# Kernel optimization log

Measured on AMD Instinct MI355X. Metric: run time of the kernel, lower is better.

## Reference

```python
import jax, jax.numpy as jnp
import numpy as np

B, N, DIM, H, E = 2, 2048, 1024, 16, 8
HD = DIM // H
SCALE = HD ** -0.5


def setup_inputs() -> dict:
    key = jax.random.key(0)
    ks = jax.random.split(key, 6)
    s = DIM ** -0.5
    return {
        "x": jax.random.normal(ks[0], (B, N, DIM), dtype=jnp.float32),
        "w_qkv": jax.random.normal(ks[1], (3 * DIM, DIM), dtype=jnp.float32) * s,
        "b_qkv": jnp.zeros((3 * DIM,), dtype=jnp.float32),
        "w_proj": jax.random.normal(ks[2], (DIM, DIM), dtype=jnp.float32) * s,
        "b_proj": jnp.zeros((DIM,), dtype=jnp.float32),
        "rel_pos": jax.random.normal(ks[3], (1, H, E, E), dtype=jnp.float32),
    }


def reference(x, w_qkv, b_qkv, w_proj, b_proj, rel_pos):
    tpe = N // E  # tokens per entity (tile count)
    # qkv: [B,N,3*DIM] -> [3,B,H,N,HD]
    qkv = (jnp.einsum("bnc,dc->bnd", x, w_qkv) + b_qkv)
    qkv = qkv.reshape(B, N, 3, H, HD).transpose(2, 0, 3, 1, 4)
    q, k, v = qkv[0], qkv[1], qkv[2]
    attn = jnp.einsum("bhnd,bhmd->bhnm", q, k) * SCALE
    # torch .repeat tiles the ExE bias: bias[i,j] = rel_pos[i % E, j % E]
    rel_bias = jnp.tile(rel_pos, (B, 1, tpe, tpe))
    attn = jax.nn.softmax(attn + rel_bias, axis=-1)
    out = jnp.einsum("bhnm,bhmd->bhnd", attn, v)
    out = out.transpose(0, 2, 1, 3).reshape(B, N, DIM)
    return jnp.einsum("bnc,dc->bnd", out, w_proj) + b_proj
```

## Files before the change

### kernel.cpp

```cpp
#include <hip/hip_runtime.h>
#include <hip/hip_bf16.h>
#include <stdint.h>

#define B_ 2
#define N_ 2048
#define DIM_ 1024
#define H_ 16
#define HD_ 64
#define NT_ 32

typedef __attribute__((ext_vector_type(8))) short short8;
typedef __attribute__((ext_vector_type(4))) float f32x4;

__device__ __forceinline__ unsigned short f2bf(float f) {
  __bf16 h = (__bf16)f;
  return __builtin_bit_cast(unsigned short, h);
}

__device__ __forceinline__ void gload_lds16(const void* g, void* l) {
  __builtin_amdgcn_global_load_lds(
      (const __attribute__((address_space(1))) unsigned int*)g,
      (__attribute__((address_space(3))) unsigned int*)l,
      16, 0, 0);
}

#define XN4_ 1048576
#define WQ4_ 786432
__global__ __launch_bounds__(256) void cvt_all_kernel(
    const float4* __restrict__ x, const float4* __restrict__ wq,
    const float4* __restrict__ wp,
    ushort4* __restrict__ xb, ushort4* __restrict__ wqb, ushort4* __restrict__ wpb) {
  int i = blockIdx.x * 256 + threadIdx.x;
  const float4* src;
  ushort4* dst;
  if (i < XN4_) {
    src = x + i; dst = xb + i;
  } else if (i < XN4_ + WQ4_) {
    src = wq + (i - XN4_); dst = wqb + (i - XN4_);
  } else {
    src = wp + (i - XN4_ - WQ4_); dst = wpb + (i - XN4_ - WQ4_);
  }
  float4 v = *src;
  ushort4 o;
  o.x = f2bf(v.x); o.y = f2bf(v.y); o.z = f2bf(v.z); o.w = f2bf(v.w);
  *dst = o;
}

__device__ __forceinline__ void gemm128_mainloop(
    const ushort* __restrict__ A, const ushort* __restrict__ Bw, int K,
    int bm, int bn, ushort* As, ushort* Bs, f32x4 acc[4][4]) {
  const int tid = threadIdx.x;
  const int lane = tid & 63;
  const int w = tid >> 6, wr = w >> 1, wc = w & 1;
  const int fr = lane & 15, fq = lane >> 4;
  const int srow = tid >> 3, scol = (tid & 7) * 8;

  const ushort* Ag = A + (size_t)(bm * 128 + srow) * K + scol;
  const ushort* Bg = Bw + (size_t)(bn * 128 + srow) * K + scol;
  ushort* Asd = As + tid * 8;
  ushort* Bsd = Bs + tid * 8;

  for (int kt = 0; kt < K; kt += 64) {
    __syncthreads();
#pragma unroll
    for (int c = 0; c < 4; ++c) {
      gload_lds16(Ag + (size_t)(c * 32) * K + kt, Asd + c * 2048);
      gload_lds16(Bg + (size_t)(c * 32) * K + kt, Bsd + c * 2048);
    }
    __syncthreads();

    short8 af[2][4], bf[2][4];
#pragma unroll
    for (int kk = 0; kk < 2; ++kk) {
#pragma unroll
      for (int mi = 0; mi < 4; ++mi)
        af[kk][mi] = *(const short8*)&As[(wr * 64 + mi * 16 + fr) * 64 + kk * 32 + fq * 8];
#pragma unroll
      for (int ni = 0; ni < 4; ++ni)
        bf[kk][ni] = *(const short8*)&Bs[(wc * 64 + ni * 16 + fr) * 64 + kk * 32 + fq * 8];
    }
#pragma unroll
    for (int kk = 0; kk < 2; ++kk)
#pragma unroll
      for (int mi = 0; mi < 4; ++mi)
#pragma unroll
        for (int ni = 0; ni < 4; ++ni)
          acc[mi][ni] = __builtin_amdgcn_mfma_f32_16x16x32_bf16(
              af[kk][mi], bf[kk][ni], acc[mi][ni], 0, 0, 0);
  }
}

__global__ __launch_bounds__(256) void gemm_qkv_kernel(
    const ushort* __restrict__ xb, const ushort* __restrict__ wqkv,
    const float* __restrict__ bqkv,
    ushort* __restrict__ qo, ushort* __restrict__ ko, ushort* __restrict__ vo) {
  __shared__ ushort As[128 * 64];
  __shared__ ushort Bs[128 * 64];
  f32x4 acc[4][4] = {};
  const int bn = blockIdx.x, bm = blockIdx.y;
  gemm128_mainloop(xb, wqkv, DIM_, bm, bn, As, Bs, acc);

  const int tid = threadIdx.x, lane = tid & 63;
  const int w = tid >> 6, wr = w >> 1, wc = w & 1;
  const int fr = lane & 15, fq = lane >> 4;
#pragma unroll
  for (int mi = 0; mi < 4; ++mi) {
#pragma unroll
    for (int ni = 0; ni < 4; ++ni) {
      int col = bn * 128 + wc * 64 + ni * 16 + fr;
      int i3 = col >> 10, h = (col >> 6) & 15, hd = col & 63;
      float bias = bqkv[col];
      int m0 = bm * 128 + wr * 64 + mi * 16 + fq * 4;
      int b = m0 >> 11, n = m0 & 2047;
      if (i3 == 2) {
        ushort4 o;
        o.x = f2bf(acc[mi][ni][0] + bias);
        o.y = f2bf(acc[mi][ni][1] + bias);
        o.z = f2bf(acc[mi][ni][2] + bias);
        o.w = f2bf(acc[mi][ni][3] + bias);
        *(ushort4*)&vo[((size_t)((b * H_ + h) * HD_ + hd)) * N_ + n] = o;
      } else {
        ushort* base = (i3 == 0) ? qo : ko;
#pragma unroll
        for (int r = 0; r < 4; ++r)
          base[((size_t)(b * H_ + h) * N_ + n + r) * HD_ + hd] = f2bf(acc[mi][ni][r] + bias);
      }
    }
  }
}

__global__ __launch_bounds__(256) void gemm_proj_kernel(
    const ushort* __restrict__ ao, const ushort* __restrict__ wp,
    const float* __restrict__ bp, float* __restrict__ out) {
  __shared__ ushort As[128 * 64];
  __shared__ ushort Bs[128 * 64];
  f32x4 acc[4][4] = {};
  const int bn = blockIdx.x, bm = blockIdx.y;
  gemm128_mainloop(ao, wp, DIM_, bm, bn, As, Bs, acc);

  const int tid = threadIdx.x, lane = tid & 63;
  const int w = tid >> 6, wr = w >> 1, wc = w & 1;
  const int fr = lane & 15, fq = lane >> 4;
#pragma unroll
  for (int mi = 0; mi < 4; ++mi) {
#pragma unroll
    for (int ni = 0; ni < 4; ++ni) {
      int col = bn * 128 + wc * 64 + ni * 16 + fr;
      float bias = bp[col];
#pragma unroll
      for (int r = 0; r < 4; ++r) {
        int m = bm * 128 + wr * 64 + mi * 16 + fq * 4 + r;
        out[(size_t)m * DIM_ + col] = acc[mi][ni][r] + bias;
      }
    }
  }
}

__global__ __launch_bounds__(256) void attn_kernel(
    const ushort* __restrict__ Qg, const ushort* __restrict__ Kg,
    const ushort* __restrict__ Vtg, const float* __restrict__ rel,
    ushort* __restrict__ outb) {
  __shared__ ushort Ks[2][64 * 64];
  __shared__ ushort Vs[2][64 * 64];
  __shared__ ushort Ps[4][2][16 * 64];

  const int bid = blockIdx.x;
  const int xcd = bid & 7, idx = bid >> 3;
  const int bh = xcd * 4 + (idx >> 4);
  const int q0 = (idx & 15) * 128;
  const int h = bh & 15;
  const int tid = threadIdx.x, lane = tid & 63, w = tid >> 6;
  const int fr = lane & 15, fq = lane >> 4;

  const float LOG2E = 1.4426950408889634f;
  const float SB = 0.125f * LOG2E;

  float bias2[4];
#pragma unroll
  for (int r = 0; r < 4; ++r)
    bias2[r] = rel[h * 64 + (fr & 7) * 8 + ((fq * 4 + r) & 7)] * LOG2E;

  short8 qf[2][2];
#pragma unroll
  for (int g = 0; g < 2; ++g) {
    const ushort* qrow = Qg + ((size_t)bh * N_ + q0 + w * 32 + g * 16 + fr) * HD_;
    qf[g][0] = *(const short8*)&qrow[fq * 8];
    qf[g][1] = *(const short8*)&qrow[32 + fq * 8];
  }

  float l_[2] = {0.f, 0.f};
  f32x4 oacc[2][4] = {};

  const int srow = tid >> 3, scol = (tid & 7) * 8;
  const int swsrc = scol ^ ((srow & 7) << 3);
  const int csw[2] = {(fq * 8) ^ ((fr & 7) << 3), (32 + fq * 8) ^ ((fr & 7) << 3)};

#define STAGE(t, b)                                                                   \
  {                                                                                   \
    const size_t kv0 = (size_t)(t) * 64;                                              \
    _Pragma("unroll") for (int c = 0; c < 2; ++c) {                                   \
      gload_lds16(Kg + ((size_t)bh * N_ + kv0 + c * 32 + srow) * HD_ + swsrc,         \
                  &Ks[b][c * 2048 + tid * 8]);                                        \
      gload_lds16(Vtg + ((size_t)(bh * HD_ + c * 32 + srow)) * N_ + kv0 + swsrc,      \
                  &Vs[b][c * 2048 + tid * 8]);                                        \
    }                                                                                 \
  }

  STAGE(0, 0);
  __syncthreads();

  for (int t = 0; t < NT_; ++t) {
    const int cur = t & 1;
    if (t + 1 < NT_) STAGE(t + 1, cur ^ 1);

    const ushort* K_ = Ks[cur];
    const ushort* V_ = Vs[cur];

    f32x4 sacc[2][4] = {};
    __builtin_amdgcn_s_setprio(1);
#pragma unroll
    for (int kk = 0; kk < 2; ++kk)
#pragma unroll
      for (int s = 0; s < 4; ++s) {
        short8 kf = *(const short8*)&K_[(s * 16 + fr) * 64 + csw[kk]];
        sacc[0][s] = __builtin_amdgcn_mfma_f32_16x16x32_bf16(kf, qf[0][kk], sacc[0][s], 0, 0, 0);
        sacc[1][s] = __builtin_amdgcn_mfma_f32_16x16x32_bf16(kf, qf[1][kk], sacc[1][s], 0, 0, 0);
      }
    __builtin_amdgcn_s_setprio(0);

#pragma unroll
    for (int g = 0; g < 2; ++g) {
      float rs = 0.f;
      ushort* pw = Ps[w][g];
#pragma unroll
      for (int s = 0; s < 4; ++s) {
        float p0 = __builtin_amdgcn_exp2f(sacc[g][s][0] * SB + bias2[0]);
        float p1 = __builtin_amdgcn_exp2f(sacc[g][s][1] * SB + bias2[1]);
        float p2 = __builtin_amdgcn_exp2f(sacc[g][s][2] * SB + bias2[2]);
        float p3 = __builtin_amdgcn_exp2f(sacc[g][s][3] * SB + bias2[3]);
        rs += (p0 + p1) + (p2 + p3);
        uint2 pk;
        pk.x = ((uint32_t)f2bf(p1) << 16) | f2bf(p0);
        pk.y = ((uint32_t)f2bf(p3) << 16) | f2bf(p2);
        *(uint2*)&pw[fr * 64 + ((s * 16 + fq * 4) ^ ((fr & 7) << 3))] = pk;
      }
      rs += __shfl_xor(rs, 16, 64);
      rs += __shfl_xor(rs, 32, 64);
      l_[g] += rs;
    }

#pragma unroll
    for (int kk = 0; kk < 2; ++kk) {
      short8 pf0 = *(const short8*)&Ps[w][0][fr * 64 + csw[kk]];
      short8 pf1 = *(const short8*)&Ps[w][1][fr * 64 + csw[kk]];
      __builtin_amdgcn_s_setprio(1);
#pragma unroll
      for (int di = 0; di < 4; ++di) {
        short8 vf = *(const short8*)&V_[(di * 16 + fr) * 64 + csw[kk]];
        oacc[0][di] = __builtin_amdgcn_mfma_f32_16x16x32_bf16(vf, pf0, oacc[0][di], 0, 0, 0);
        oacc[1][di] = __builtin_amdgcn_mfma_f32_16x16x32_bf16(vf, pf1, oacc[1][di], 0, 0, 0);
      }
      __builtin_amdgcn_s_setprio(0);
    }
    __syncthreads();
  }

  const int b = bh >> 4;
#pragma unroll
  for (int g = 0; g < 2; ++g) {
    float invl = 1.0f / l_[g];
    size_t rowbase = ((size_t)(b * N_ + q0 + w * 32 + g * 16 + fr)) * DIM_ + h * HD_;
#pragma unroll
    for (int di = 0; di < 4; ++di) {
      ushort4 o;
      o.x = f2bf(oacc[g][di][0] * invl);
      o.y = f2bf(oacc[g][di][1] * invl);
      o.z = f2bf(oacc[g][di][2] * invl);
      o.w = f2bf(oacc[g][di][3] * invl);
      *(ushort4*)&outb[rowbase + di * 16 + fq * 4] = o;
    }
  }
#undef STAGE
}

extern "C" void kernel_launch(void* const* d_in, const int* in_sizes, int n_in,
                              void* d_out, int out_size, void* d_ws, size_t ws_size,
                              hipStream_t stream) {
  const float* x      = (const float*)d_in[0];
  const float* w_qkv  = (const float*)d_in[1];
  const float* b_qkv  = (const float*)d_in[2];
  const float* w_proj = (const float*)d_in[3];
  const float* b_proj = (const float*)d_in[4];
  const float* rel    = (const float*)d_in[5];

  char* ws = (char*)d_ws;
  ushort* xb     = (ushort*)(ws + 0);
  ushort* wqkvb  = (ushort*)(ws + 8388608);
  ushort* wprojb = (ushort*)(ws + 14680064);
  ushort* qb     = (ushort*)(ws + 16777216);
  ushort* kb     = (ushort*)(ws + 25165824);
  ushort* vb     = (ushort*)(ws + 33554432);
  ushort* aob    = (ushort*)(ws + 41943040);
  (void)in_sizes; (void)n_in; (void)out_size; (void)ws_size;

  cvt_all_kernel<<<8192, 256, 0, stream>>>(
      (const float4*)x, (const float4*)w_qkv, (const float4*)w_proj,
      (ushort4*)xb, (ushort4*)wqkvb, (ushort4*)wprojb);

  gemm_qkv_kernel<<<dim3(24, 32), 256, 0, stream>>>(xb, wqkvb, b_qkv, qb, kb, vb);
  attn_kernel<<<512, 256, 0, stream>>>(qb, kb, vb, rel, aob);
  gemm_proj_kernel<<<dim3(8, 32), 256, 0, stream>>>(aob, wprojb, b_proj, (float*)d_out);
}
```

Measured before the change: 146.0 us.

## Use 32x32 MFMA with register-resident P and software-pipelined QK/PV in attention

Rewrites the attention inner loop around 32x32x16 bf16 MFMAs. The softmax probabilities stay in registers, rearranged with v_permlane32_swap, instead of going through an LDS round trip. K and V staging are split, and the loop is software-pipelined so the QK^T of the next tile is issued alongside the softmax and PV of the current one. The aim is to remove the P LDS writes and reads, cut MFMA issue count, and overlap exp work with matrix work, at the cost of more registers, since two score accumulators are live (launch bounds set to 2).

```diff
diff --git a/kernel.cpp b/kernel.cpp
--- a/kernel.cpp
+++ b/kernel.cpp
@@ -11,6 +11,7 @@
 
 typedef __attribute__((ext_vector_type(8))) short short8;
 typedef __attribute__((ext_vector_type(4))) float f32x4;
+typedef __attribute__((ext_vector_type(16))) float f32x16;
 
 __device__ __forceinline__ unsigned short f2bf(float f) {
   __bf16 h = (__bf16)f;
@@ -156,13 +157,12 @@
   }
 }
 
-__global__ __launch_bounds__(256) void attn_kernel(
+__global__ __launch_bounds__(256, 2) void attn_kernel(
     const ushort* __restrict__ Qg, const ushort* __restrict__ Kg,
     const ushort* __restrict__ Vtg, const float* __restrict__ rel,
     ushort* __restrict__ outb) {
   __shared__ ushort Ks[2][64 * 64];
   __shared__ ushort Vs[2][64 * 64];
-  __shared__ ushort Ps[4][2][16 * 64];
 
   const int bid = blockIdx.x;
   const int xcd = bid & 7, idx = bid >> 3;
@@ -170,7 +170,7 @@
   const int q0 = (idx & 15) * 128;
   const int h = bh & 15;
   const int tid = threadIdx.x, lane = tid & 63, w = tid >> 6;
-  const int fr = lane & 15, fq = lane >> 4;
+  const int ql = lane & 31, hi = lane >> 5;
 
   const float LOG2E = 1.4426950408889634f;
   const float SB = 0.125f * LOG2E;
@@ -178,109 +178,133 @@
   float bias2[4];
 #pragma unroll
   for (int r = 0; r < 4; ++r)
-    bias2[r] = rel[h * 64 + (fr & 7) * 8 + ((fq * 4 + r) & 7)] * LOG2E;
-
-  short8 qf[2][2];
-#pragma unroll
-  for (int g = 0; g < 2; ++g) {
-    const ushort* qrow = Qg + ((size_t)bh * N_ + q0 + w * 32 + g * 16 + fr) * HD_;
-    qf[g][0] = *(const short8*)&qrow[fq * 8];
-    qf[g][1] = *(const short8*)&qrow[32 + fq * 8];
-  }
-
-  float l_[2] = {0.f, 0.f};
-  f32x4 oacc[2][4] = {};
+    bias2[r] = rel[h * 64 + (ql & 7) * 8 + r + 4 * hi] * LOG2E;
+
+  const ushort* qrow = Qg + ((size_t)bh * N_ + q0 + w * 32 + ql) * HD_;
+  short8 qf[4];
+#pragma unroll
+  for (int kk = 0; kk < 4; ++kk)
+    qf[kk] = *(const short8*)&qrow[kk * 16 + hi * 8];
+
+  float l = 0.f;
+  f32x16 oacc[2] = {};
+  f32x16 sA[2], sB[2];
 
   const int srow = tid >> 3, scol = (tid & 7) * 8;
   const int swsrc = scol ^ ((srow & 7) << 3);
-  const int csw[2] = {(fq * 8) ^ ((fr & 7) << 3), (32 + fq * 8) ^ ((fr & 7) << 3)};
-
-#define STAGE(t, b)                                                                   \
-  {                                                                                   \
-    const size_t kv0 = (size_t)(t) * 64;                                              \
-    _Pragma("unroll") for (int c = 0; c < 2; ++c) {                                   \
-      gload_lds16(Kg + ((size_t)bh * N_ + kv0 + c * 32 + srow) * HD_ + swsrc,         \
-                  &Ks[b][c * 2048 + tid * 8]);                                        \
-      gload_lds16(Vtg + ((size_t)(bh * HD_ + c * 32 + srow)) * N_ + kv0 + swsrc,      \
-                  &Vs[b][c * 2048 + tid * 8]);                                        \
-    }                                                                                 \
-  }
-
-  STAGE(0, 0);
+  int kcol[4];
+#pragma unroll
+  for (int kk = 0; kk < 4; ++kk)
+    kcol[kk] = (kk * 16 + hi * 8) ^ ((ql & 7) << 3);
+
+#define STAGE_K(t, bb)                                                              \
+  {                                                                                 \
+    const size_t kv0 = (size_t)(t) * 64;                                            \
+    _Pragma("unroll") for (int c = 0; c < 2; ++c)                                   \
+        gload_lds16(Kg + ((size_t)bh * N_ + kv0 + c * 32 + srow) * HD_ + swsrc,     \
+                    &Ks[bb][c * 2048 + tid * 8]);                                   \
+  }
+#define STAGE_V(t, bb)                                                              \
+  {                                                                                 \
+    const size_t kv0 = (size_t)(t) * 64;                                            \
+    _Pragma("unroll") for (int c = 0; c < 2; ++c)                                   \
+        gload_lds16(Vtg + ((size_t)(bh * HD_ + c * 32 + srow)) * N_ + kv0 + swsrc,  \
+                    &Vs[bb][c * 2048 + tid * 8]);                                   \
+  }
+
+#define QKT(S, K_)                                                                  \
+  {                                                                                 \
+    _Pragma("unroll") for (int z = 0; z < 16; ++z) { S[0][z] = 0.f; S[1][z] = 0.f; }\
+    __builtin_amdgcn_s_setprio(1);                                                  \
+    _Pragma("unroll") for (int kk = 0; kk < 4; ++kk) {                              \
+      short8 kf0 = *(const short8*)&(K_)[ql * 64 + kcol[kk]];                       \
+      short8 kf1 = *(const short8*)&(K_)[(32 + ql) * 64 + kcol[kk]];                \
+      S[0] = __builtin_amdgcn_mfma_f32_32x32x16_bf16(kf0, qf[kk], S[0], 0, 0, 0);   \
+      S[1] = __builtin_amdgcn_mfma_f32_32x32x16_bf16(kf1, qf[kk], S[1], 0, 0, 0);   \
+    }                                                                               \
+    __builtin_amdgcn_s_setprio(0);                                                  \
+  }
+
+#define SOFTPV(S, V_)                                                               \
+  {                                                                                 \
+    float rs = 0.f;                                                                 \
+    uint32_t c[2][8];                                                               \
+    _Pragma("unroll") for (int blk = 0; blk < 2; ++blk) {                           \
+      _Pragma("unroll") for (int i = 0; i < 8; ++i) {                               \
+        float pa = __builtin_amdgcn_exp2f(S[blk][2 * i] * SB + bias2[(2 * i) & 3]); \
+        float pb = __builtin_amdgcn_exp2f(S[blk][2 * i + 1] * SB + bias2[(2 * i + 1) & 3]); \
+        rs += pa + pb;                                                              \
+        c[blk][i] = ((uint32_t)f2bf(pb) << 16) | f2bf(pa);                          \
+      }                                                                             \
+    }                                                                               \
+    rs += __shfl_xor(rs, 32, 64);                                                   \
+    l += rs;                                                                        \
+    _Pragma("unroll") for (int blk = 0; blk < 2; ++blk) {                           \
+      asm("v_permlane32_swap_b32 %0, %1" : "+v"(c[blk][0]), "+v"(c[blk][2]));       \
+      asm("v_permlane32_swap_b32 %0, %1" : "+v"(c[blk][1]), "+v"(c[blk][3]));       \
+      asm("v_permlane32_swap_b32 %0, %1" : "+v"(c[blk][4]), "+v"(c[blk][6]));       \
+      asm("v_permlane32_swap_b32 %0, %1" : "+v"(c[blk][5]), "+v"(c[blk][7]));       \
+    }                                                                               \
+    __builtin_amdgcn_s_setprio(1);                                                  \
+    _Pragma("unroll") for (int kk = 0; kk < 4; ++kk) {                              \
+      union { uint32_t u[4]; short8 s8; } pb_;                                      \
+      pb_.u[0] = c[kk >> 1][(kk & 1) * 4 + 0];                                      \
+      pb_.u[1] = c[kk >> 1][(kk & 1) * 4 + 1];                                      \
+      pb_.u[2] = c[kk >> 1][(kk & 1) * 4 + 2];                                      \
+      pb_.u[3] = c[kk >> 1][(kk & 1) * 4 + 3];                                      \
+      _Pragma("unroll") for (int db = 0; db < 2; ++db) {                            \
+        short8 vf = *(const short8*)&(V_)[(db * 32 + ql) * 64 + kcol[kk]];          \
+        oacc[db] = __builtin_amdgcn_mfma_f32_32x32x16_bf16(vf, pb_.s8, oacc[db], 0, 0, 0); \
+      }                                                                             \
+    }                                                                               \
+    __builtin_amdgcn_s_setprio(0);                                                  \
+  }
+
+  STAGE_K(0, 0);
+  STAGE_V(0, 0);
   __syncthreads();
-
-  for (int t = 0; t < NT_; ++t) {
-    const int cur = t & 1;
-    if (t + 1 < NT_) STAGE(t + 1, cur ^ 1);
-
-    const ushort* K_ = Ks[cur];
-    const ushort* V_ = Vs[cur];
-
-    f32x4 sacc[2][4] = {};
-    __builtin_amdgcn_s_setprio(1);
-#pragma unroll
-    for (int kk = 0; kk < 2; ++kk)
-#pragma unroll
-      for (int s = 0; s < 4; ++s) {
-        short8 kf = *(const short8*)&K_[(s * 16 + fr) * 64 + csw[kk]];
-        sacc[0][s] = __builtin_amdgcn_mfma_f32_16x16x32_bf16(kf, qf[0][kk], sacc[0][s], 0, 0, 0);
-        sacc[1][s] = __builtin_amdgcn_mfma_f32_16x16x32_bf16(kf, qf[1][kk], sacc[1][s], 0, 0, 0);
-      }
-    __builtin_amdgcn_s_setprio(0);
-
-#pragma unroll
-    for (int g = 0; g < 2; ++g) {
-      float rs = 0.f;
-      ushort* pw = Ps[w][g];
-#pragma unroll
-      for (int s = 0; s < 4; ++s) {
-        float p0 = __builtin_amdgcn_exp2f(sacc[g][s][0] * SB + bias2[0]);
-        float p1 = __builtin_amdgcn_exp2f(sacc[g][s][1] * SB + bias2[1]);
-        float p2 = __builtin_amdgcn_exp2f(sacc[g][s][2] * SB + bias2[2]);
-        float p3 = __builtin_amdgcn_exp2f(sacc[g][s][3] * SB + bias2[3]);
-        rs += (p0 + p1) + (p2 + p3);
-        uint2 pk;
-        pk.x = ((uint32_t)f2bf(p1) << 16) | f2bf(p0);
-        pk.y = ((uint32_t)f2bf(p3) << 16) | f2bf(p2);
-        *(uint2*)&pw[fr * 64 + ((s * 16 + fq * 4) ^ ((fr & 7) << 3))] = pk;
-      }
-      rs += __shfl_xor(rs, 16, 64);
-      rs += __shfl_xor(rs, 32, 64);
-      l_[g] += rs;
-    }
-
-#pragma unroll
-    for (int kk = 0; kk < 2; ++kk) {
-      short8 pf0 = *(const short8*)&Ps[w][0][fr * 64 + csw[kk]];
-      short8 pf1 = *(const short8*)&Ps[w][1][fr * 64 + csw[kk]];
-      __builtin_amdgcn_s_setprio(1);
-#pragma unroll
-      for (int di = 0; di < 4; ++di) {
-        short8 vf = *(const short8*)&V_[(di * 16 + fr) * 64 + csw[kk]];
-        oacc[0][di] = __builtin_amdgcn_mfma_f32_16x16x32_bf16(vf, pf0, oacc[0][di], 0, 0, 0);
-        oacc[1][di] = __builtin_amdgcn_mfma_f32_16x16x32_bf16(vf, pf1, oacc[1][di], 0, 0, 0);
-      }
-      __builtin_amdgcn_s_setprio(0);
-    }
+  QKT(sA, Ks[0]);
+  STAGE_K(1, 1);
+  __syncthreads();
+
+#pragma unroll 1
+  for (int tt = 0; tt < 15; ++tt) {
+    const int t = 2 * tt;
+    STAGE_K(t + 2, 0);
+    STAGE_V(t + 1, 1);
+    QKT(sB, Ks[1]);
+    SOFTPV(sA, Vs[0]);
     __syncthreads();
-  }
+    STAGE_K(t + 3, 1);
+    STAGE_V(t + 2, 0);
+    QKT(sA, Ks[0]);
+    SOFTPV(sB, Vs[1]);
+    __syncthreads();
+  }
+  STAGE_V(31, 1);
+  QKT(sB, Ks[1]);
+  SOFTPV(sA, Vs[0]);
+  __syncthreads();
+  SOFTPV(sB, Vs[1]);
 
   const int b = bh >> 4;
-#pragma unroll
-  for (int g = 0; g < 2; ++g) {
-    float invl = 1.0f / l_[g];
-    size_t rowbase = ((size_t)(b * N_ + q0 + w * 32 + g * 16 + fr)) * DIM_ + h * HD_;
-#pragma unroll
-    for (int di = 0; di < 4; ++di) {
+  const float invl = 1.0f / l;
+  const size_t rowbase = ((size_t)(b * N_ + q0 + w * 32 + ql)) * DIM_ + h * HD_;
+#pragma unroll
+  for (int db = 0; db < 2; ++db)
+#pragma unroll
+    for (int g = 0; g < 4; ++g) {
       ushort4 o;
-      o.x = f2bf(oacc[g][di][0] * invl);
-      o.y = f2bf(oacc[g][di][1] * invl);
-      o.z = f2bf(oacc[g][di][2] * invl);
-      o.w = f2bf(oacc[g][di][3] * invl);
-      *(ushort4*)&outb[rowbase + di * 16 + fq * 4] = o;
-    }
-  }
-#undef STAGE
+      o.x = f2bf(oacc[db][4 * g + 0] * invl);
+      o.y = f2bf(oacc[db][4 * g + 1] * invl);
+      o.z = f2bf(oacc[db][4 * g + 2] * invl);
+      o.w = f2bf(oacc[db][4 * g + 3] * invl);
+      *(ushort4*)&outb[rowbase + db * 32 + 8 * g + 4 * hi] = o;
+    }
+#undef STAGE_K
+#undef STAGE_V
+#undef QKT
+#undef SOFTPV
 }
 
 extern "C" void kernel_launch(void* const* d_in, const int* in_sizes, int n_in,
```

Result: faster. 137.8 us (-5.6%).
